# Performance work log

Measured on AMD Instinct MI355X. Metric: run time of the kernel, lower is better.

## Reference

```python
import jax, jax.numpy as jnp
import numpy as np

KERNEL_MUL = 2.0
KERNEL_NUM = 5
ZERO_SUM_FILL = 100.0  # original replaces zero class-sums with 100 before dividing


def _cal_weight(s_label, t_label):
    # s_label, t_label: [B, C]; normalize each class column by its batch mass,
    # zero out classes absent in either domain (faithful to intended semantics).
    s_sum = jnp.sum(s_label, axis=0, keepdims=True)           # [1, C]
    t_sum = jnp.sum(t_label, axis=0, keepdims=True)           # [1, C]
    s_vec = s_label / jnp.where(s_sum == 0, ZERO_SUM_FILL, s_sum)
    t_vec = t_label / jnp.where(t_sum == 0, ZERO_SUM_FILL, t_sum)
    valid = ((s_sum != 0) & (t_sum != 0)).astype(s_label.dtype)  # [1, C]
    s_vec = s_vec * valid
    t_vec = t_vec * valid
    w_ss = s_vec @ s_vec.T   # [B, B]
    w_tt = t_vec @ t_vec.T   # [B, B]
    w_st = s_vec @ t_vec.T   # [B, B]
    return w_ss, w_tt, w_st


def _multi_kernel(source, target):
    n = source.shape[0] + target.shape[0]
    total = jnp.concatenate([source, target], axis=0)          # [N, D]
    # pairwise squared L2 via GEMM trick: same math as (x_i - x_j)^2 summed over D
    sq = jnp.sum(total * total, axis=1)                        # [N]
    l2 = sq[:, None] + sq[None, :] - 2.0 * (total @ total.T)   # [N, N]
    # bandwidth from detached distances (median-like heuristic)
    bw = jax.lax.stop_gradient(jnp.sum(l2)) / (n * n - n)
    bw = bw / (KERNEL_MUL ** (KERNEL_NUM // 2))
    kernels = jnp.zeros_like(l2)
    for i in range(KERNEL_NUM):
        kernels = kernels + jnp.exp(-l2 / (bw * (KERNEL_MUL ** i)))
    return kernels


def setup_inputs() -> dict:
    key = jax.random.key(0)
    k1, k2, k3, k4 = jax.random.split(key, 4)
    B, D, C = 4096, 256, 31
    return {
        "source": jax.random.normal(k1, (B, D), dtype=jnp.float32),
        "target": jax.random.normal(k2, (B, D), dtype=jnp.float32),
        "s_label": jax.random.uniform(k3, (B, C), dtype=jnp.float32),
        "t_label": jax.random.uniform(k4, (B, C), dtype=jnp.float32),
    }


def reference(source, target, s_label, t_label):
    B = source.shape[0]
    # weights are computed in numpy in the original -> constants w.r.t. grads
    w_ss, w_tt, w_st = _cal_weight(jax.lax.stop_gradient(s_label),
                                   jax.lax.stop_gradient(t_label))
    kernels = _multi_kernel(source, target)                    # [2B, 2B]
    SS = kernels[:B, :B]
    TT = kernels[B:, B:]
    ST = kernels[:B, B:]
    loss = jnp.sum(w_ss * SS + w_tt * TT - 2.0 * w_st * ST)
    return loss.reshape(1)
```

## Files before the change

### kernel.cpp

```cpp
#include <hip/hip_runtime.h>
#include <hip/hip_bf16.h>
#include <math.h>

#define BN 4096
#define DD 256
#define CC 31
#define KP 352
#define AUGA 256
#define AUGB 288
#define LABK 320
#define LROW 40

typedef __attribute__((ext_vector_type(8))) short bf16x8;
typedef __attribute__((ext_vector_type(4))) float f32x4;

static __device__ inline unsigned short f2bf(float v) {
  __hip_bfloat16 h = __float2bfloat16(v);
  union { __hip_bfloat16 h; unsigned short u; } cv;
  cv.h = h;
  return cv.u;
}
static __device__ inline float bf2f(unsigned short u) {
  return __uint_as_float(((unsigned int)u) << 16);
}


__global__ void stats_kernel(const float* __restrict__ source,
                             const float* __restrict__ target,
                             const float* __restrict__ s_label,
                             const float* __restrict__ t_label,
                             double* __restrict__ colsum,
                             double* __restrict__ sumsq,
                             double* __restrict__ labsumS,
                             double* __restrict__ labsumT) {
  const int d = threadIdx.x;
  const int r0 = blockIdx.x * 32;
  float cs = 0.f, sq = 0.f;
  for (int r = r0; r < r0 + 32; ++r) {
    const float v = (r < BN) ? source[(size_t)r * DD + d]
                             : target[(size_t)(r - BN) * DD + d];
    cs += v;
    sq += v * v;
  }
  atomicAdd(&colsum[d], (double)cs);
  __shared__ float red[256];
  red[d] = sq;
  __syncthreads();
  for (int s = 128; s; s >>= 1) {
    if (d < s) red[d] += red[d + s];
    __syncthreads();
  }
  if (d == 0) atomicAdd(sumsq, (double)red[0]);

  if (d < CC) {
    const bool isS = (blockIdx.x < 128);
    const int lr0 = (isS ? blockIdx.x : blockIdx.x - 128) * 32;
    const float* lab = isS ? s_label : t_label;
    float ls = 0.f;
    for (int r = lr0; r < lr0 + 32; ++r) ls += lab[(size_t)r * CC + d];
    atomicAdd(isS ? &labsumS[d] : &labsumT[d], (double)ls);
  }
}

__global__ void bw_scale_kernel(const double* __restrict__ sumsq,
                                const double* __restrict__ colsum,
                                const double* __restrict__ labsumS,
                                const double* __restrict__ labsumT,
                                float* __restrict__ negc,
                                float* __restrict__ aScale,
                                float* __restrict__ bScale) {
  __shared__ double red[256];
  int t = threadIdx.x;
  double cs = colsum[t];
  red[t] = cs * cs;
  __syncthreads();
  for (int s = 128; s; s >>= 1) {
    if (t < s) red[t] += red[t + s];
    __syncthreads();
  }
  if (t == 0) {
    double suml2 = 2.0 * 8192.0 * (*sumsq) - 2.0 * red[0];
    double bw = suml2 / (8192.0 * 8192.0 - 8192.0);
    bw = bw / 4.0;
    for (int k = 0; k < 5; ++k)
      negc[k] = (float)(-1.0 / (bw * (double)(1 << k)));
  }
  if (t < 32) {
    double s_sum = (t < CC) ? labsumS[t] : 0.0;
    double t_sum = (t < CC) ? labsumT[t] : 0.0;
    bool valid = (t < CC) && (s_sum != 0.0) && (t_sum != 0.0);
    aScale[t] = valid ? (float)(1.0 / s_sum) : 0.f;
    bScale[t] = valid ? (float)(1.0 / t_sum) : 0.f;
  }
}

__global__ void pack_kernel(const float* __restrict__ source,
                            const float* __restrict__ target,
                            const float* __restrict__ s_label,
                            const float* __restrict__ t_label,
                            const float* __restrict__ aScale,
                            const float* __restrict__ bScale,
                            unsigned short* __restrict__ pack) {
  const int vr = blockIdx.x * 4 + (threadIdx.x >> 6);
  const int l = threadIdx.x & 63;
  const bool isS = (vr < BN);
  const float* xp = isS ? (source + (size_t)vr * DD)
                        : (target + (size_t)(vr - BN) * DD);
  float4 v = ((const float4*)xp)[l];
  unsigned short ub[4] = {f2bf(v.x), f2bf(v.y), f2bf(v.z), f2bf(v.w)};
  float f[4];
#pragma unroll
  for (int e = 0; e < 4; ++e) f[e] = bf2f(ub[e]);
  float sq = f[0] * f[0] + f[1] * f[1] + f[2] * f[2] + f[3] * f[3];
#pragma unroll
  for (int off = 32; off; off >>= 1) sq += __shfl_xor(sq, off);

  const size_t rb = (size_t)vr * KP;
  *(short4*)&pack[rb + l * 4] =
      make_short4((short)ub[0], (short)ub[1], (short)ub[2], (short)ub[3]);

  if (l < 8) {
    const unsigned short one = f2bf(1.0f);
    const float hs = -0.5f * sq;
    const unsigned short hh = f2bf(hs);
    const unsigned short lo = f2bf(hs - bf2f(hh));
    const int c0 = l * 4;
    unsigned short a_aug[4], b_aug[4], labv[4];
#pragma unroll
    for (int e = 0; e < 4; ++e) {
      const int c = c0 + e;
      a_aug[e] = (c == 0) ? hh : (c == 1) ? lo : (c <= 3) ? one : (unsigned short)0;
      b_aug[e] = (c <= 1) ? one : (c == 2) ? hh : (c == 3) ? lo : (unsigned short)0;
      float lv = 0.f;
      if (c < CC) {
        lv = isS ? s_label[(size_t)vr * CC + c] * aScale[c]
                 : t_label[(size_t)(vr - BN) * CC + c] * bScale[c];
      }
      labv[e] = f2bf(lv);
    }
    *(short4*)&pack[rb + AUGA + c0] = make_short4(
        (short)a_aug[0], (short)a_aug[1], (short)a_aug[2], (short)a_aug[3]);
    *(short4*)&pack[rb + AUGB + c0] = make_short4(
        (short)b_aug[0], (short)b_aug[1], (short)b_aug[2], (short)b_aug[3]);
    *(short4*)&pack[rb + LABK + c0] = make_short4(
        (short)labv[0], (short)labv[1], (short)labv[2], (short)labv[3]);
  }
}

__global__ __launch_bounds__(256) void lmmd_main(
    const unsigned short* __restrict__ pack, const float* __restrict__ negc,
    double* __restrict__ accOut) {
  __shared__ __align__(16) unsigned short bufB[2][128][LROW];
  __shared__ double dred[256];

  const int t = threadIdx.x;
  const int lane = t & 63;
  const int wv = t >> 6;
  const int bi = blockIdx.x >> 6;
  const int bj = blockIdx.x & 63;
  const int r15 = lane & 15;
  const int kb0 = (lane >> 4) * 8;

  const int rowSi = (bi * 64 + wv * 16 + r15) * KP;
  const int rowTi = rowSi + BN * KP;

  const int srow = t >> 1;
  const int soff = (t & 1) * 16;
  const int srowG = (srow < 64) ? (bj * 64 + srow) : (BN + bj * 64 + (srow - 64));
  const size_t sbase = (size_t)srowG * KP;

  constexpr int koAarr[10] = {0, 32, 64, 96, 128, 160, 192, 224, AUGA, LABK};
  constexpr int koBarr[10] = {0, 32, 64, 96, 128, 160, 192, 224, AUGB, LABK};

  f32x4 aSS[4], aTT[4], aST[4], wSS[4], wTT[4], wST[4];
#pragma unroll
  for (int n = 0; n < 4; ++n) {
    aSS[n] = {0.f, 0.f, 0.f, 0.f};
    aTT[n] = {0.f, 0.f, 0.f, 0.f};
    aST[n] = {0.f, 0.f, 0.f, 0.f};
    wSS[n] = {0.f, 0.f, 0.f, 0.f};
    wTT[n] = {0.f, 0.f, 0.f, 0.f};
    wST[n] = {0.f, 0.f, 0.f, 0.f};
  }

  {
    const float4 v0 = *(const float4*)&pack[sbase + koBarr[0] + soff];
    const float4 v1 = *(const float4*)&pack[sbase + koBarr[0] + soff + 8];
    *(float4*)&bufB[0][srow][soff] = v0;
    *(float4*)&bufB[0][srow][soff + 8] = v1;
  }

#pragma unroll
  for (int c = 0; c < 10; ++c) {
    __syncthreads();
    float4 s0, s1;
    if (c < 9) {
      s0 = *(const float4*)&pack[sbase + koBarr[c + 1] + soff];
      s1 = *(const float4*)&pack[sbase + koBarr[c + 1] + soff + 8];
    }
    const bf16x8 aS = *(const bf16x8*)&pack[rowSi + koAarr[c] + kb0];
    const bf16x8 aT = *(const bf16x8*)&pack[rowTi + koAarr[c] + kb0];
    const int cb = c & 1;
#pragma unroll
    for (int n = 0; n < 4; ++n) {
      const bf16x8 bS = *(const bf16x8*)&bufB[cb][n * 16 + r15][kb0];
      const bf16x8 bT = *(const bf16x8*)&bufB[cb][64 + n * 16 + r15][kb0];
      if (c < 9) {
        aSS[n] = __builtin_amdgcn_mfma_f32_16x16x32_bf16(aS, bS, aSS[n], 0, 0, 0);
        aTT[n] = __builtin_amdgcn_mfma_f32_16x16x32_bf16(aT, bT, aTT[n], 0, 0, 0);
        aST[n] = __builtin_amdgcn_mfma_f32_16x16x32_bf16(aS, bT, aST[n], 0, 0, 0);
      } else {
        wSS[n] = __builtin_amdgcn_mfma_f32_16x16x32_bf16(aS, bS, wSS[n], 0, 0, 0);
        wTT[n] = __builtin_amdgcn_mfma_f32_16x16x32_bf16(aT, bT, wTT[n], 0, 0, 0);
        wST[n] = __builtin_amdgcn_mfma_f32_16x16x32_bf16(aS, bT, wST[n], 0, 0, 0);
      }
    }
    if (c < 9) {
      const int nb = (c + 1) & 1;
      *(float4*)&bufB[nb][srow][soff] = s0;
      *(float4*)&bufB[nb][srow][soff + 8] = s1;
    }
  }

  const float nc0 = negc[0], nc1 = negc[1], nc2 = negc[2], nc3 = negc[3],
              nc4 = negc[4];
  double tsum = 0.0;
#pragma unroll
  for (int n = 0; n < 4; ++n) {
#pragma unroll
    for (int e = 0; e < 4; ++e) {
      const float l2ss = -2.f * aSS[n][e];
      const float l2tt = -2.f * aTT[n][e];
      const float l2st = -2.f * aST[n][e];
      const float Kss = __expf(l2ss * nc0) + __expf(l2ss * nc1) +
                        __expf(l2ss * nc2) + __expf(l2ss * nc3) +
                        __expf(l2ss * nc4);
      const float Ktt = __expf(l2tt * nc0) + __expf(l2tt * nc1) +
                        __expf(l2tt * nc2) + __expf(l2tt * nc3) +
                        __expf(l2tt * nc4);
      const float Kst = __expf(l2st * nc0) + __expf(l2st * nc1) +
                        __expf(l2st * nc2) + __expf(l2st * nc3) +
                        __expf(l2st * nc4);
      tsum += (double)(wSS[n][e] * Kss + wTT[n][e] * Ktt -
                       2.f * wST[n][e] * Kst);
    }
  }
  dred[t] = tsum;
  __syncthreads();
  for (int s = 128; s; s >>= 1) {
    if (t < s) dred[t] += dred[t + s];
    __syncthreads();
  }
  if (t == 0) atomicAdd(accOut, dred[0]);
}

__global__ void finalize_kernel(const double* __restrict__ acc,
                                float* __restrict__ out) {
  out[0] = (float)acc[0];
}

extern "C" void kernel_launch(void* const* d_in, const int* in_sizes, int n_in,
                              void* d_out, int out_size, void* d_ws,
                              size_t ws_size, hipStream_t stream) {
  const float* source = (const float*)d_in[0];
  const float* target = (const float*)d_in[1];
  const float* s_label = (const float*)d_in[2];
  const float* t_label = (const float*)d_in[3];

  double* acc = (double*)d_ws;
  double* sumsq = acc + 1;
  double* colsum = acc + 2;
  double* labsumS = acc + 258;
  double* labsumT = acc + 290;
  float* fbase = (float*)((char*)d_ws + 2624);
  float* aScale = fbase;
  float* bScale = fbase + 32;
  float* negc = fbase + 64;
  unsigned short* pack = (unsigned short*)((char*)d_ws + 4096);

  hipMemsetAsync(d_ws, 0, 2624, stream);
  stats_kernel<<<256, 256, 0, stream>>>(source, target, s_label, t_label,
                                        colsum, sumsq, labsumS, labsumT);
  bw_scale_kernel<<<1, 256, 0, stream>>>(sumsq, colsum, labsumS, labsumT,
                                         negc, aScale, bScale);
  pack_kernel<<<2048, 256, 0, stream>>>(source, target, s_label, t_label,
                                        aScale, bScale, pack);
  lmmd_main<<<4096, 256, 0, stream>>>(pack, negc, acc);
  finalize_kernel<<<1, 1, 0, stream>>>(acc, (float*)d_out);
}
```

Measured before the change: 166.2 us.

## Exploit pair-kernel symmetry to skip lower-triangle tiles and fuse small kernels

The main kernel now computes only upper-triangle block tiles (bi<=bj) and doubles off-diagonal contributions. Each tile adds a TS product so the ST cross term still covers both orderings. This roughly halves the MFMA and exp work. The bandwidth/scale computation is folded into the stats kernel using a last-block counter, and finalize is folded into the main kernel the same way, which removes two launches. LDS row padding is also removed (40 to 32), which may bring back bank conflicts.

```diff
diff --git a/kernel.cpp b/kernel.cpp
--- a/kernel.cpp
+++ b/kernel.cpp
@@ -9,7 +9,6 @@
 #define AUGA 256
 #define AUGB 288
 #define LABK 320
-#define LROW 40
 
 typedef __attribute__((ext_vector_type(8))) short bf16x8;
 typedef __attribute__((ext_vector_type(4))) float f32x4;
@@ -32,7 +31,11 @@
                              double* __restrict__ colsum,
                              double* __restrict__ sumsq,
                              double* __restrict__ labsumS,
-                             double* __restrict__ labsumT) {
+                             double* __restrict__ labsumT,
+                             int* __restrict__ counter1,
+                             float* __restrict__ negc,
+                             float* __restrict__ aScale,
+                             float* __restrict__ bScale) {
   const int d = threadIdx.x;
   const int r0 = blockIdx.x * 32;
   float cs = 0.f, sq = 0.f;
@@ -60,37 +63,38 @@
     for (int r = lr0; r < lr0 + 32; ++r) ls += lab[(size_t)r * CC + d];
     atomicAdd(isS ? &labsumS[d] : &labsumT[d], (double)ls);
   }
-}
-
-__global__ void bw_scale_kernel(const double* __restrict__ sumsq,
-                                const double* __restrict__ colsum,
-                                const double* __restrict__ labsumS,
-                                const double* __restrict__ labsumT,
-                                float* __restrict__ negc,
-                                float* __restrict__ aScale,
-                                float* __restrict__ bScale) {
-  __shared__ double red[256];
-  int t = threadIdx.x;
-  double cs = colsum[t];
-  red[t] = cs * cs;
+
+  __shared__ int amLast;
+  __syncthreads();
+  if (d == 0) {
+    __threadfence();
+    amLast = (atomicAdd(counter1, 1) == 255) ? 1 : 0;
+  }
+  __syncthreads();
+  if (!amLast) return;
+
+  __shared__ double red2[256];
+  double cv = atomicAdd(&colsum[d], 0.0);
+  red2[d] = cv * cv;
   __syncthreads();
   for (int s = 128; s; s >>= 1) {
-    if (t < s) red[t] += red[t + s];
+    if (d < s) red2[d] += red2[d + s];
     __syncthreads();
   }
-  if (t == 0) {
-    double suml2 = 2.0 * 8192.0 * (*sumsq) - 2.0 * red[0];
+  if (d == 0) {
+    double ss = atomicAdd(sumsq, 0.0);
+    double suml2 = 2.0 * 8192.0 * ss - 2.0 * red2[0];
     double bw = suml2 / (8192.0 * 8192.0 - 8192.0);
     bw = bw / 4.0;
     for (int k = 0; k < 5; ++k)
       negc[k] = (float)(-1.0 / (bw * (double)(1 << k)));
   }
-  if (t < 32) {
-    double s_sum = (t < CC) ? labsumS[t] : 0.0;
-    double t_sum = (t < CC) ? labsumT[t] : 0.0;
-    bool valid = (t < CC) && (s_sum != 0.0) && (t_sum != 0.0);
-    aScale[t] = valid ? (float)(1.0 / s_sum) : 0.f;
-    bScale[t] = valid ? (float)(1.0 / t_sum) : 0.f;
+  if (d < 32) {
+    double s_sum = (d < CC) ? atomicAdd(&labsumS[d], 0.0) : 0.0;
+    double t_sum = (d < CC) ? atomicAdd(&labsumT[d], 0.0) : 0.0;
+    bool valid = (d < CC) && (s_sum != 0.0) && (t_sum != 0.0);
+    aScale[d] = valid ? (float)(1.0 / s_sum) : 0.f;
+    bScale[d] = valid ? (float)(1.0 / t_sum) : 0.f;
   }
 }
 
@@ -149,15 +153,28 @@
 
 __global__ __launch_bounds__(256) void lmmd_main(
     const unsigned short* __restrict__ pack, const float* __restrict__ negc,
-    double* __restrict__ accOut) {
-  __shared__ __align__(16) unsigned short bufB[2][128][LROW];
+    double* __restrict__ accOut, int* __restrict__ counter2,
+    float* __restrict__ out) {
+  const int t = threadIdx.x;
+  const int bi = blockIdx.x >> 6;
+  const int bj = blockIdx.x & 63;
+
+  if (bi > bj) {
+    if (t == 0) {
+      __threadfence();
+      if (atomicAdd(counter2, 1) == 4095) {
+        double v = atomicAdd(accOut, 0.0);
+        out[0] = (float)v;
+      }
+    }
+    return;
+  }
+
+  __shared__ __align__(16) unsigned short bufB[2][128][32];
   __shared__ double dred[256];
 
-  const int t = threadIdx.x;
   const int lane = t & 63;
   const int wv = t >> 6;
-  const int bi = blockIdx.x >> 6;
-  const int bj = blockIdx.x & 63;
   const int r15 = lane & 15;
   const int kb0 = (lane >> 4) * 8;
 
@@ -172,15 +189,17 @@
   constexpr int koAarr[10] = {0, 32, 64, 96, 128, 160, 192, 224, AUGA, LABK};
   constexpr int koBarr[10] = {0, 32, 64, 96, 128, 160, 192, 224, AUGB, LABK};
 
-  f32x4 aSS[4], aTT[4], aST[4], wSS[4], wTT[4], wST[4];
+  f32x4 aSS[4], aTT[4], aST1[4], aST2[4], wSS[4], wTT[4], wST1[4], wST2[4];
 #pragma unroll
   for (int n = 0; n < 4; ++n) {
     aSS[n] = {0.f, 0.f, 0.f, 0.f};
     aTT[n] = {0.f, 0.f, 0.f, 0.f};
-    aST[n] = {0.f, 0.f, 0.f, 0.f};
+    aST1[n] = {0.f, 0.f, 0.f, 0.f};
+    aST2[n] = {0.f, 0.f, 0.f, 0.f};
     wSS[n] = {0.f, 0.f, 0.f, 0.f};
     wTT[n] = {0.f, 0.f, 0.f, 0.f};
-    wST[n] = {0.f, 0.f, 0.f, 0.f};
+    wST1[n] = {0.f, 0.f, 0.f, 0.f};
+    wST2[n] = {0.f, 0.f, 0.f, 0.f};
   }
 
   {
@@ -208,11 +227,13 @@
       if (c < 9) {
         aSS[n] = __builtin_amdgcn_mfma_f32_16x16x32_bf16(aS, bS, aSS[n], 0, 0, 0);
         aTT[n] = __builtin_amdgcn_mfma_f32_16x16x32_bf16(aT, bT, aTT[n], 0, 0, 0);
-        aST[n] = __builtin_amdgcn_mfma_f32_16x16x32_bf16(aS, bT, aST[n], 0, 0, 0);
+        aST1[n] = __builtin_amdgcn_mfma_f32_16x16x32_bf16(aS, bT, aST1[n], 0, 0, 0);
+        aST2[n] = __builtin_amdgcn_mfma_f32_16x16x32_bf16(aT, bS, aST2[n], 0, 0, 0);
       } else {
         wSS[n] = __builtin_amdgcn_mfma_f32_16x16x32_bf16(aS, bS, wSS[n], 0, 0, 0);
         wTT[n] = __builtin_amdgcn_mfma_f32_16x16x32_bf16(aT, bT, wTT[n], 0, 0, 0);
-        wST[n] = __builtin_amdgcn_mfma_f32_16x16x32_bf16(aS, bT, wST[n], 0, 0, 0);
+        wST1[n] = __builtin_amdgcn_mfma_f32_16x16x32_bf16(aS, bT, wST1[n], 0, 0, 0);
+        wST2[n] = __builtin_amdgcn_mfma_f32_16x16x32_bf16(aT, bS, wST2[n], 0, 0, 0);
       }
     }
     if (c < 9) {
@@ -231,32 +252,39 @@
     for (int e = 0; e < 4; ++e) {
       const float l2ss = -2.f * aSS[n][e];
       const float l2tt = -2.f * aTT[n][e];
-      const float l2st = -2.f * aST[n][e];
+      const float l2s1 = -2.f * aST1[n][e];
+      const float l2s2 = -2.f * aST2[n][e];
       const float Kss = __expf(l2ss * nc0) + __expf(l2ss * nc1) +
                         __expf(l2ss * nc2) + __expf(l2ss * nc3) +
                         __expf(l2ss * nc4);
       const float Ktt = __expf(l2tt * nc0) + __expf(l2tt * nc1) +
                         __expf(l2tt * nc2) + __expf(l2tt * nc3) +
                         __expf(l2tt * nc4);
-      const float Kst = __expf(l2st * nc0) + __expf(l2st * nc1) +
-                        __expf(l2st * nc2) + __expf(l2st * nc3) +
-                        __expf(l2st * nc4);
+      const float Ks1 = __expf(l2s1 * nc0) + __expf(l2s1 * nc1) +
+                        __expf(l2s1 * nc2) + __expf(l2s1 * nc3) +
+                        __expf(l2s1 * nc4);
+      const float Ks2 = __expf(l2s2 * nc0) + __expf(l2s2 * nc1) +
+                        __expf(l2s2 * nc2) + __expf(l2s2 * nc3) +
+                        __expf(l2s2 * nc4);
       tsum += (double)(wSS[n][e] * Kss + wTT[n][e] * Ktt -
-                       2.f * wST[n][e] * Kst);
-    }
-  }
+                       wST1[n][e] * Ks1 - wST2[n][e] * Ks2);
+    }
+  }
+  if (bi != bj) tsum *= 2.0;
   dred[t] = tsum;
   __syncthreads();
   for (int s = 128; s; s >>= 1) {
     if (t < s) dred[t] += dred[t + s];
     __syncthreads();
   }
-  if (t == 0) atomicAdd(accOut, dred[0]);
-}
-
-__global__ void finalize_kernel(const double* __restrict__ acc,
-                                float* __restrict__ out) {
-  out[0] = (float)acc[0];
+  if (t == 0) {
+    atomicAdd(accOut, dred[0]);
+    __threadfence();
+    if (atomicAdd(counter2, 1) == 4095) {
+      double v = atomicAdd(accOut, 0.0);
+      out[0] = (float)v;
+    }
+  }
 }
 
 extern "C" void kernel_launch(void* const* d_in, const int* in_sizes, int n_in,
@@ -272,6 +300,8 @@
   double* colsum = acc + 2;
   double* labsumS = acc + 258;
   double* labsumT = acc + 290;
+  int* counter1 = (int*)((char*)d_ws + 2576);
+  int* counter2 = (int*)((char*)d_ws + 2580);
   float* fbase = (float*)((char*)d_ws + 2624);
   float* aScale = fbase;
   float* bScale = fbase + 32;
@@ -280,11 +310,10 @@
 
   hipMemsetAsync(d_ws, 0, 2624, stream);
   stats_kernel<<<256, 256, 0, stream>>>(source, target, s_label, t_label,
-                                        colsum, sumsq, labsumS, labsumT);
-  bw_scale_kernel<<<1, 256, 0, stream>>>(sumsq, colsum, labsumS, labsumT,
-                                         negc, aScale, bScale);
+                                        colsum, sumsq, labsumS, labsumT,
+                                        counter1, negc, aScale, bScale);
   pack_kernel<<<2048, 256, 0, stream>>>(source, target, s_label, t_label,
                                         aScale, bScale, pack);
-  lmmd_main<<<4096, 256, 0, stream>>>(pack, negc, acc);
-  finalize_kernel<<<1, 1, 0, stream>>>(acc, (float*)d_out);
-}
+  lmmd_main<<<4096, 256, 0, stream>>>(pack, negc, acc, counter2,
+                                      (float*)d_out);
+}
```

New measurement: 213.6 us. 28.5% more time.
